# Optimization experiments

Hardware: AMD Instinct MI355X
Metric: run time of the kernel (lower is better)

The kernel has to match this reference:

```python
import jax, jax.numpy as jnp
import numpy as np

# Block-sparse causal local attention (DeepSpeed SparseSelfAttention math):
#   scores = SDD(Q, K^T) on nonzero layout blocks
#   scores = masked_fill(block-causal mask == 0, -inf)
#   probs  = sparse_softmax(scores * head_dim**-0.5)  (rpe=None, key_padding_mask=None)
#   out    = DSD(probs, V)
# Layout: block (i, j) is nonzero iff 0 <= i - j < W (causal sliding window of W blocks).

BSZ, H, S, D = 2, 8, 4096, 64
BLK = 32          # sparsity block size
W = 16            # number of local key blocks per query block (512-token window)


def setup_inputs() -> dict:
    key = jax.random.key(0)
    kq, kk, kv = jax.random.split(key, 3)
    query = jax.random.normal(kq, (BSZ, H, S, D), jnp.float32)
    k = jax.random.normal(kk, (BSZ, H, S, D), jnp.float32)
    v = jax.random.normal(kv, (BSZ, H, S, D), jnp.float32)
    return {"query": query, "key": k, "value": v}


def reference(query, key, value):
    b, h, s, d = query.shape
    nb = s // BLK
    scaling = float(d) ** -0.5

    qb = query.reshape(b, h, nb, BLK, d)
    kb = key.reshape(b, h, nb, BLK, d)
    vb = value.reshape(b, h, nb, BLK, d)

    blk_i = jnp.arange(nb)
    # key-block indices attended by each query block: i-W+1 ... i   [nb, W]
    k_idx = blk_i[:, None] + jnp.arange(-(W - 1), 1)[None, :]
    blk_valid = k_idx >= 0
    k_idx_c = jnp.maximum(k_idx, 0)

    Kg = kb[:, :, k_idx_c]   # [b, h, nb, W, BLK, d]
    Vg = vb[:, :, k_idx_c]   # [b, h, nb, W, BLK, d]

    # block-sparse SDD: only the W local blocks per query block are computed
    scores = jnp.einsum('bhnqd,bhnwkd->bhnqwk', qb, Kg) * scaling

    # token-level causal mask (covers the diagonal-block triangular mask
    # from make_sparse_attn_mask) + validity of gathered blocks
    qpos = blk_i[:, None] * BLK + jnp.arange(BLK)[None, :]           # [nb, BLK]
    kpos = k_idx_c[..., None] * BLK + jnp.arange(BLK)                # [nb, W, BLK]
    allowed = blk_valid[:, None, :, None] & (kpos[:, None, :, :] <= qpos[:, :, None, None])
    scores = jnp.where(allowed[None, None], scores, -jnp.inf)

    # fused sparse softmax over all present key positions of each query row
    probs = jax.nn.softmax(scores.reshape(b, h, nb, BLK, W * BLK), axis=-1)
    probs = probs.reshape(b, h, nb, BLK, W, BLK)

    # block-sparse DSD
    out = jnp.einsum('bhnqwk,bhnwkd->bhnqd', probs, Vg)
    return out.reshape(b, h, s, d)
```

## Files before the change

kernel.cpp:

```cpp
#include <hip/hip_runtime.h>
#include <hip/hip_bf16.h>


#define NH    8
#define SEQ   4096
#define DIM   64
#define NBLK  128
#define WIN   16
#define QG    4
#define GROUPS (NBLK / QG)

typedef __bf16 bf16x8 __attribute__((ext_vector_type(8)));
typedef __bf16 bf16x4 __attribute__((ext_vector_type(4)));
typedef float  f32x4  __attribute__((ext_vector_type(4)));
typedef float  f32x2  __attribute__((ext_vector_type(2)));
typedef unsigned short u16;
typedef unsigned int   u32;

#define KSTR 72
#define VSTR 40
#define DTHR 8.0f

__device__ __forceinline__ bf16x4 cvt4(f32x4 a) {
    bf16x4 r;
#pragma unroll
    for (int j = 0; j < 4; ++j) r[j] = (__bf16)a[j];
    return r;
}

__global__ __launch_bounds__(512)
void sparse_attn_v19(const float* __restrict__ Q,
                     const float* __restrict__ K,
                     const float* __restrict__ V,
                     float* __restrict__ O)
{
    const int b  = (int)blockIdx.x;
    const int lg = (b & 7) * 64 + (b >> 3);
    const int bh = lg >> 5;
    const int n0 = (lg & 31) * QG;

    const int t    = (int)threadIdx.x;
    const int wave = t >> 6;
    const int lane = t & 63;
    const int l15  = lane & 15;
    const int l4   = lane >> 4;
    const int qi   = wave >> 1;
    const int rh   = wave & 1;
    const int nq   = n0 + qi;

    __shared__ u16 Kt[2][32][KSTR];
    __shared__ u16 Vt[2][64][VSTR];

    const size_t base = (size_t)bh * SEQ * DIM;
    const float SC = 0.125f * 1.44269504088896340736f;

    const int skrow = t >> 4;
    const int skc   = (t & 15) * 4;
    const int svkey = (t & 15) * 2;
    const int svd2  = t >> 4;
    const int vp    = (svkey & 3) | (((svkey >> 2) & 3) << 3) | ((svkey >> 4) << 2);

    bf16x8 qf[2];
    {
        const float* qp = Q + base + (size_t)(nq * 32 + rh * 16 + l15) * DIM + l4 * 8;
        f32x4 a0 = *(const f32x4*)qp        * SC;
        f32x4 b0 = *(const f32x4*)(qp + 4)  * SC;
        f32x4 a1 = *(const f32x4*)(qp + 32) * SC;
        f32x4 b1 = *(const f32x4*)(qp + 36) * SC;
#pragma unroll
        for (int j = 0; j < 4; ++j) {
            qf[0][j] = (__bf16)a0[j]; qf[0][4 + j] = (__bf16)b0[j];
            qf[1][j] = (__bf16)a1[j]; qf[1][4 + j] = (__bf16)b1[j];
        }
    }

    f32x4 acc[4] = {};
    float m  = -1e30f;
    float lp = 0.f;

    const int lo  = (nq >= WIN - 1) ? nq - (WIN - 1) : 0;
    const int kb0 = (n0 >= WIN - 1) ? n0 - (WIN - 1) : 0;
    const int kb1 = n0 + QG - 1;

    f32x4 kr;  f32x2 va, vb;
    {
        const float* kp = K + base + (size_t)(kb0 * 32 + skrow) * DIM + skc;
        kr = *(const f32x4*)kp;
        const float* vptr = V + base + (size_t)(kb0 * 32 + svkey) * DIM + svd2 * 2;
        va = *(const f32x2*)vptr;
        vb = *(const f32x2*)(vptr + DIM);
    }
    {
        *(bf16x4*)&Kt[0][skrow][skc] = cvt4(kr);
#pragma unroll
        for (int j = 0; j < 2; ++j) {
            u32 w = (u32)__builtin_bit_cast(u16, (__bf16)va[j])
                  | ((u32)__builtin_bit_cast(u16, (__bf16)vb[j]) << 16);
            *(u32*)&Vt[0][svd2 * 2 + j][vp] = w;
        }
    }
    __syncthreads();

    int cur = 0;
    for (int kb = kb0; kb <= kb1; ++kb) {
        {
            const int kn = (kb + 1 <= kb1) ? kb + 1 : kb1;
            const float* kp = K + base + (size_t)(kn * 32 + skrow) * DIM + skc;
            kr = *(const f32x4*)kp;
            const float* vptr = V + base + (size_t)(kn * 32 + svkey) * DIM + svd2 * 2;
            va = *(const f32x2*)vptr;
            vb = *(const f32x2*)(vptr + DIM);
        }

        if (kb >= lo && kb <= nq) {
            bf16x8 kf[2][2];
#pragma unroll
            for (int kh = 0; kh < 2; ++kh)
#pragma unroll
                for (int c = 0; c < 2; ++c)
                    kf[kh][c] = *(const bf16x8*)&Kt[cur][kh * 16 + l15][c * 32 + l4 * 8];

            bf16x8 vf[4];
#pragma unroll
            for (int dt = 0; dt < 4; ++dt)
                vf[dt] = *(const bf16x8*)&Vt[cur][dt * 16 + l15][l4 * 8];

            f32x4 s[2];
#pragma unroll
            for (int kh = 0; kh < 2; ++kh) {
                f32x4 a = {};
                a = __builtin_amdgcn_mfma_f32_16x16x32_bf16(kf[kh][0], qf[0], a, 0, 0, 0);
                a = __builtin_amdgcn_mfma_f32_16x16x32_bf16(kf[kh][1], qf[1], a, 0, 0, 0);
                s[kh] = a;
            }

            if (kb == nq) {
#pragma unroll
                for (int kh = 0; kh < 2; ++kh)
#pragma unroll
                    for (int r = 0; r < 4; ++r)
                        if (kh * 16 + l4 * 4 + r > rh * 16 + l15)
                            s[kh][r] = -1e30f;
            }

            bool ok = true;
#pragma unroll
            for (int kh = 0; kh < 2; ++kh)
#pragma unroll
                for (int r = 0; r < 4; ++r)
                    ok &= (s[kh][r] <= m + DTHR);

            if (!__all(ok)) {
                float t0 = -1e30f;
#pragma unroll
                for (int kh = 0; kh < 2; ++kh)
#pragma unroll
                    for (int r = 0; r < 4; ++r) t0 = fmaxf(t0, s[kh][r]);
                t0 = fmaxf(t0, __shfl_xor(t0, 16));
                t0 = fmaxf(t0, __shfl_xor(t0, 32));
                const float mn = fmaxf(m, t0);
                const float al = exp2f(m - mn);
                m = mn;
                lp *= al;
#pragma unroll
                for (int dt = 0; dt < 4; ++dt)
#pragma unroll
                    for (int r = 0; r < 4; ++r) acc[dt][r] *= al;
            }

            bf16x8 pbf;
            float psum = 0.f;
#pragma unroll
            for (int j = 0; j < 8; ++j) {
                const float pv = exp2f(s[j >> 2][j & 3] - m);
                psum += pv;
                pbf[j] = (__bf16)pv;
            }
            lp += psum;

#pragma unroll
            for (int dt = 0; dt < 4; ++dt)
                acc[dt] = __builtin_amdgcn_mfma_f32_16x16x32_bf16(
                    vf[dt], pbf, acc[dt], 0, 0, 0);
        }

        {
            *(bf16x4*)&Kt[cur ^ 1][skrow][skc] = cvt4(kr);
#pragma unroll
            for (int j = 0; j < 2; ++j) {
                u32 w = (u32)__builtin_bit_cast(u16, (__bf16)va[j])
                      | ((u32)__builtin_bit_cast(u16, (__bf16)vb[j]) << 16);
                *(u32*)&Vt[cur ^ 1][svd2 * 2 + j][vp] = w;
            }
        }

        __syncthreads();
        cur ^= 1;
    }

    {
        float ps = lp;
        ps += __shfl_xor(ps, 16);
        ps += __shfl_xor(ps, 32);
        const float inv = 1.0f / ps;
        float* op = O + base + (size_t)(nq * 32 + rh * 16 + l15) * DIM + l4 * 4;
#pragma unroll
        for (int dt = 0; dt < 4; ++dt) {
            f32x4 v;
#pragma unroll
            for (int r = 0; r < 4; ++r) v[r] = acc[dt][r] * inv;
            *(f32x4*)(op + dt * 16) = v;
        }
    }
}

extern "C" void kernel_launch(void* const* d_in, const int* in_sizes, int n_in,
                              void* d_out, int out_size, void* d_ws, size_t ws_size,
                              hipStream_t stream)
{
    const float* Q = (const float*)d_in[0];
    const float* K = (const float*)d_in[1];
    const float* V = (const float*)d_in[2];
    float*       O = (float*)d_out;

    const int nwg = 2 * NH * GROUPS;
    hipLaunchKernelGGL(sparse_attn_v19, dim3(nwg), dim3(512), 0, stream,
                       Q, K, V, O);
}
```

Before: 33.95 us.

## Deepen K/V prefetch to two blocks with fixed-trip unrolled loop and lighter barrier

Restructures the key-block loop so global loads run two blocks ahead in alternating register sets. The loop now has a fixed trip count of 19 blocks, with negative block indices clamped and skipped by the compute guard, and is unrolled by two so the LDS buffer index is a compile-time constant. __syncthreads is replaced by an explicit lgkmcnt wait plus s_barrier, with sched_barriers around it, so the barrier does not wait on outstanding vector-memory loads. The aim is to hide global latency better. In exchange, edge groups do useless load iterations and register pressure goes up.

```diff
diff --git a/kernel.cpp b/kernel.cpp
--- a/kernel.cpp
+++ b/kernel.cpp
@@ -29,7 +29,7 @@
 }
 
 __global__ __launch_bounds__(512)
-void sparse_attn_v19(const float* __restrict__ Q,
+void sparse_attn_v20(const float* __restrict__ Q,
                      const float* __restrict__ K,
                      const float* __restrict__ V,
                      float* __restrict__ O)
@@ -79,124 +79,124 @@
     float lp = 0.f;
 
     const int lo  = (nq >= WIN - 1) ? nq - (WIN - 1) : 0;
-    const int kb0 = (n0 >= WIN - 1) ? n0 - (WIN - 1) : 0;
+    const int kb0 = n0 - (WIN - 1);
     const int kb1 = n0 + QG - 1;
 
-    f32x4 kr;  f32x2 va, vb;
-    {
-        const float* kp = K + base + (size_t)(kb0 * 32 + skrow) * DIM + skc;
-        kr = *(const f32x4*)kp;
-        const float* vptr = V + base + (size_t)(kb0 * 32 + svkey) * DIM + svd2 * 2;
-        va = *(const f32x2*)vptr;
-        vb = *(const f32x2*)(vptr + DIM);
-    }
-    {
-        *(bf16x4*)&Kt[0][skrow][skc] = cvt4(kr);
-#pragma unroll
-        for (int j = 0; j < 2; ++j) {
-            u32 w = (u32)__builtin_bit_cast(u16, (__bf16)va[j])
-                  | ((u32)__builtin_bit_cast(u16, (__bf16)vb[j]) << 16);
-            *(u32*)&Vt[0][svd2 * 2 + j][vp] = w;
-        }
-    }
-    __syncthreads();
-
-    int cur = 0;
-    for (int kb = kb0; kb <= kb1; ++kb) {
+#define LOADB(KB, KR, VA, VB)                                                   \
+    { int kn_ = (KB); kn_ = (kn_ < 0) ? 0 : ((kn_ > kb1) ? kb1 : kn_);          \
+      const float* kp_ = K + base + (size_t)(kn_ * 32 + skrow) * DIM + skc;     \
+      KR = *(const f32x4*)kp_;                                                  \
+      const float* vp_ = V + base + (size_t)(kn_ * 32 + svkey) * DIM + svd2 * 2;\
+      VA = *(const f32x2*)vp_;  VB = *(const f32x2*)(vp_ + DIM); }
+
+#define STOREB(CUR, KR, VA, VB)                                                 \
+    { *(bf16x4*)&Kt[CUR][skrow][skc] = cvt4(KR);                                \
+      _Pragma("unroll")                                                         \
+      for (int j = 0; j < 2; ++j) {                                             \
+          u32 w_ = (u32)__builtin_bit_cast(u16, (__bf16)VA[j])                  \
+                 | ((u32)__builtin_bit_cast(u16, (__bf16)VB[j]) << 16);         \
+          *(u32*)&Vt[CUR][svd2 * 2 + j][vp] = w_; } }
+
+#define LITEBAR()                                                               \
+    { asm volatile("s_waitcnt lgkmcnt(0)" ::: "memory");                        \
+      __builtin_amdgcn_sched_barrier(0);                                        \
+      __builtin_amdgcn_s_barrier();                                             \
+      __builtin_amdgcn_sched_barrier(0); }
+
+#define COMPUTE(KB, CUR)                                                        \
+    if ((KB) >= lo && (KB) <= nq) {                                             \
+        bf16x8 kf[2][2];                                                        \
+        _Pragma("unroll")                                                       \
+        for (int kh = 0; kh < 2; ++kh)                                          \
+            _Pragma("unroll")                                                   \
+            for (int c = 0; c < 2; ++c)                                         \
+                kf[kh][c] = *(const bf16x8*)&Kt[CUR][kh * 16 + l15][c * 32 + l4 * 8]; \
+        bf16x8 vf[4];                                                           \
+        _Pragma("unroll")                                                       \
+        for (int dt = 0; dt < 4; ++dt)                                          \
+            vf[dt] = *(const bf16x8*)&Vt[CUR][dt * 16 + l15][l4 * 8];           \
+        f32x4 s[2];                                                             \
+        _Pragma("unroll")                                                       \
+        for (int kh = 0; kh < 2; ++kh) {                                        \
+            f32x4 a = {};                                                       \
+            a = __builtin_amdgcn_mfma_f32_16x16x32_bf16(kf[kh][0], qf[0], a, 0, 0, 0); \
+            a = __builtin_amdgcn_mfma_f32_16x16x32_bf16(kf[kh][1], qf[1], a, 0, 0, 0); \
+            s[kh] = a;                                                          \
+        }                                                                       \
+        if ((KB) == nq) {                                                       \
+            _Pragma("unroll")                                                   \
+            for (int kh = 0; kh < 2; ++kh)                                      \
+                _Pragma("unroll")                                               \
+                for (int r = 0; r < 4; ++r)                                     \
+                    if (kh * 16 + l4 * 4 + r > rh * 16 + l15)                   \
+                        s[kh][r] = -1e30f;                                      \
+        }                                                                       \
+        bool ok = true;                                                         \
+        _Pragma("unroll")                                                       \
+        for (int kh = 0; kh < 2; ++kh)                                          \
+            _Pragma("unroll")                                                   \
+            for (int r = 0; r < 4; ++r)                                         \
+                ok &= (s[kh][r] <= m + DTHR);                                   \
+        if (!__all(ok)) {                                                       \
+            float t0 = -1e30f;                                                  \
+            _Pragma("unroll")                                                   \
+            for (int kh = 0; kh < 2; ++kh)                                      \
+                _Pragma("unroll")                                               \
+                for (int r = 0; r < 4; ++r) t0 = fmaxf(t0, s[kh][r]);           \
+            t0 = fmaxf(t0, __shfl_xor(t0, 16));                                 \
+            t0 = fmaxf(t0, __shfl_xor(t0, 32));                                 \
+            const float mn = fmaxf(m, t0);                                      \
+            const float al = exp2f(m - mn);                                     \
+            m = mn;                                                             \
+            lp *= al;                                                           \
+            _Pragma("unroll")                                                   \
+            for (int dt = 0; dt < 4; ++dt)                                      \
+                _Pragma("unroll")                                               \
+                for (int r = 0; r < 4; ++r) acc[dt][r] *= al;                   \
+        }                                                                       \
+        bf16x8 pbf;                                                            \
+        float psum = 0.f;                                                       \
+        _Pragma("unroll")                                                       \
+        for (int j = 0; j < 8; ++j) {                                           \
+            const float pv = exp2f(s[j >> 2][j & 3] - m);                       \
+            psum += pv;                                                         \
+            pbf[j] = (__bf16)pv;                                                \
+        }                                                                       \
+        lp += psum;                                                             \
+        _Pragma("unroll")                                                       \
+        for (int dt = 0; dt < 4; ++dt)                                          \
+            acc[dt] = __builtin_amdgcn_mfma_f32_16x16x32_bf16(                  \
+                vf[dt], pbf, acc[dt], 0, 0, 0);                                 \
+    }
+
+    f32x4 krA, krB;  f32x2 vaA, vbA, vaB, vbB;
+    LOADB(kb0,     krA, vaA, vbA)
+    LOADB(kb0 + 1, krB, vaB, vbB)
+    STOREB(0, krA, vaA, vbA)
+    LITEBAR()
+
+    for (int p = 0; p < 18; p += 2) {
         {
-            const int kn = (kb + 1 <= kb1) ? kb + 1 : kb1;
-            const float* kp = K + base + (size_t)(kn * 32 + skrow) * DIM + skc;
-            kr = *(const f32x4*)kp;
-            const float* vptr = V + base + (size_t)(kn * 32 + svkey) * DIM + svd2 * 2;
-            va = *(const f32x2*)vptr;
-            vb = *(const f32x2*)(vptr + DIM);
-        }
-
-        if (kb >= lo && kb <= nq) {
-            bf16x8 kf[2][2];
-#pragma unroll
-            for (int kh = 0; kh < 2; ++kh)
-#pragma unroll
-                for (int c = 0; c < 2; ++c)
-                    kf[kh][c] = *(const bf16x8*)&Kt[cur][kh * 16 + l15][c * 32 + l4 * 8];
-
-            bf16x8 vf[4];
-#pragma unroll
-            for (int dt = 0; dt < 4; ++dt)
-                vf[dt] = *(const bf16x8*)&Vt[cur][dt * 16 + l15][l4 * 8];
-
-            f32x4 s[2];
-#pragma unroll
-            for (int kh = 0; kh < 2; ++kh) {
-                f32x4 a = {};
-                a = __builtin_amdgcn_mfma_f32_16x16x32_bf16(kf[kh][0], qf[0], a, 0, 0, 0);
-                a = __builtin_amdgcn_mfma_f32_16x16x32_bf16(kf[kh][1], qf[1], a, 0, 0, 0);
-                s[kh] = a;
-            }
-
-            if (kb == nq) {
-#pragma unroll
-                for (int kh = 0; kh < 2; ++kh)
-#pragma unroll
-                    for (int r = 0; r < 4; ++r)
-                        if (kh * 16 + l4 * 4 + r > rh * 16 + l15)
-                            s[kh][r] = -1e30f;
-            }
-
-            bool ok = true;
-#pragma unroll
-            for (int kh = 0; kh < 2; ++kh)
-#pragma unroll
-                for (int r = 0; r < 4; ++r)
-                    ok &= (s[kh][r] <= m + DTHR);
-
-            if (!__all(ok)) {
-                float t0 = -1e30f;
-#pragma unroll
-                for (int kh = 0; kh < 2; ++kh)
-#pragma unroll
-                    for (int r = 0; r < 4; ++r) t0 = fmaxf(t0, s[kh][r]);
-                t0 = fmaxf(t0, __shfl_xor(t0, 16));
-                t0 = fmaxf(t0, __shfl_xor(t0, 32));
-                const float mn = fmaxf(m, t0);
-                const float al = exp2f(m - mn);
-                m = mn;
-                lp *= al;
-#pragma unroll
-                for (int dt = 0; dt < 4; ++dt)
-#pragma unroll
-                    for (int r = 0; r < 4; ++r) acc[dt][r] *= al;
-            }
-
-            bf16x8 pbf;
-            float psum = 0.f;
-#pragma unroll
-            for (int j = 0; j < 8; ++j) {
-                const float pv = exp2f(s[j >> 2][j & 3] - m);
-                psum += pv;
-                pbf[j] = (__bf16)pv;
-            }
-            lp += psum;
-
-#pragma unroll
-            for (int dt = 0; dt < 4; ++dt)
-                acc[dt] = __builtin_amdgcn_mfma_f32_16x16x32_bf16(
-                    vf[dt], pbf, acc[dt], 0, 0, 0);
-        }
-
+            const int kb_p = kb0 + p;
+            LOADB(kb_p + 2, krA, vaA, vbA)
+            COMPUTE(kb_p, 0)
+            STOREB(1, krB, vaB, vbB)
+            LITEBAR()
+        }
         {
-            *(bf16x4*)&Kt[cur ^ 1][skrow][skc] = cvt4(kr);
-#pragma unroll
-            for (int j = 0; j < 2; ++j) {
-                u32 w = (u32)__builtin_bit_cast(u16, (__bf16)va[j])
-                      | ((u32)__builtin_bit_cast(u16, (__bf16)vb[j]) << 16);
-                *(u32*)&Vt[cur ^ 1][svd2 * 2 + j][vp] = w;
-            }
-        }
-
-        __syncthreads();
-        cur ^= 1;
-    }
+            const int kb_p = kb0 + p + 1;
+            LOADB(kb_p + 2, krB, vaB, vbB)
+            COMPUTE(kb_p, 1)
+            STOREB(0, krA, vaA, vbA)
+            LITEBAR()
+        }
+    }
+    COMPUTE(kb1, 0)
+
+#undef LOADB
+#undef STOREB
+#undef LITEBAR
+#undef COMPUTE
 
     {
         float ps = lp;
@@ -224,6 +224,6 @@
     float*       O = (float*)d_out;
 
     const int nwg = 2 * NH * GROUPS;
-    hipLaunchKernelGGL(sparse_attn_v19, dim3(nwg), dim3(512), 0, stream,
+    hipLaunchKernelGGL(sparse_attn_v20, dim3(nwg), dim3(512), 0, stream,
                        Q, K, V, O);
 }
```

Result: no change. 33.52 us (-1.3%).
